# Optimization experiments

Hardware: AMD Instinct MI355X
Metric: run time of the kernel (lower is better)

## Reference

```python
import jax, jax.numpy as jnp
import numpy as np

N = 8192
IN_F = 512
OUT_F = 64
ALPHA = 0.2  # LeakyReLU negative slope
NEG_INF = -9e15


def setup_inputs() -> dict:
    key = jax.random.key(0)
    k1, k2, k3, k4 = jax.random.split(key, 4)
    # xavier_uniform-style scale (gain=1.414)
    w_bound = 1.414 * np.sqrt(6.0 / (IN_F + OUT_F))
    a_bound = 1.414 * np.sqrt(6.0 / (2 * OUT_F + 1))
    return {
        "input": jax.random.normal(k1, (N, IN_F), dtype=jnp.float32),
        "adj": jax.random.randint(k2, (N, N), 0, 2, dtype=jnp.int32),
        "W": jax.random.uniform(k3, (IN_F, OUT_F), jnp.float32, -w_bound, w_bound),
        "a": jax.random.uniform(k4, (2 * OUT_F, 1), jnp.float32, -a_bound, a_bound),
        "sig_sample_size": 512,
    }


def reference(input, adj, W, a, sig_sample_size):
    h = input @ W  # [N, F]
    # Split 'a' so e_ij = leakyrelu(a1.h_i + a2.h_j) without the N*N*2F repeat/cat
    a1, a2 = a[:OUT_F, 0], a[OUT_F:, 0]  # [F], [F]
    e = jax.nn.leaky_relu((h @ a1)[:, None] + (h @ a2)[None, :], negative_slope=ALPHA)  # [N, N]
    attention = jnp.where(adj > 0, e, NEG_INF)
    attention = jax.nn.softmax(attention, axis=1)
    sig_scores = jnp.sum(attention, axis=0)  # [N]
    _, indices = jax.lax.top_k(sig_scores, sig_sample_size)
    return indices
```

## Files before the change

kernel.cpp:

```cpp
#include <hip/hip_runtime.h>
#include <stdint.h>

#define NROW 8192
#define IN_F 512
#define OUT_F 64
#define ALPHA 0.2f

typedef int int4e __attribute__((ext_vector_type(4)));

__device__ float  g_wa1[IN_F];
__device__ float  g_wa2[IN_F];
__device__ float  g_f1[NROW];
__device__ float  g_f2[NROW];
__device__ float  g_E2f[NROW];
__device__ float  g_F2f[NROW];
__device__ double g_E2d[NROW];
__device__ double g_F2d[NROW];
__device__ double g_accp[NROW];
__device__ double g_accn[NROW];
__device__ double g_colsum[NROW];
__device__ unsigned long long g_maskP[(size_t)NROW * 128];
__device__ unsigned long long g_maskN[(size_t)NROW * 128];

__global__ void prep_wa(const float* __restrict__ W, const float* __restrict__ a) {
    int k = threadIdx.x;
    if (k < IN_F) {
        double s1 = 0.0, s2 = 0.0;
        for (int t = 0; t < OUT_F; ++t) {
            double w = (double)W[k * OUT_F + t];
            s1 += w * (double)a[t];
            s2 += w * (double)a[OUT_F + t];
        }
        g_wa1[k] = (float)s1;
        g_wa2[k] = (float)s2;
        #pragma unroll
        for (int i = 0; i < 16; ++i) g_colsum[k * 16 + i] = 0.0;
    }
}

__global__ void __launch_bounds__(256) compute_f(const float* __restrict__ in) {
    int wave = threadIdx.x >> 6, lane = threadIdx.x & 63;
    int row = blockIdx.x * 4 + wave;
    const float4* in4  = (const float4*)(in + (size_t)row * IN_F);
    const float4* wa14 = (const float4*)g_wa1;
    const float4* wa24 = (const float4*)g_wa2;
    double s1 = 0.0, s2 = 0.0;
    #pragma unroll
    for (int half = 0; half < 2; ++half) {
        int idx = half * 64 + lane;
        float4 x = in4[idx];
        float4 u = wa14[idx];
        float4 v = wa24[idx];
        s1 += (double)x.x*u.x + (double)x.y*u.y + (double)x.z*u.z + (double)x.w*u.w;
        s2 += (double)x.x*v.x + (double)x.y*v.y + (double)x.z*v.z + (double)x.w*v.w;
    }
    #pragma unroll
    for (int off = 32; off > 0; off >>= 1) {
        s1 += __shfl_down(s1, off, 64);
        s2 += __shfl_down(s2, off, 64);
    }
    if (lane == 0) {
        float f1 = (float)s1, f2 = (float)s2;
        g_f1[row] = f1; g_f2[row] = f2;
        double e2 = exp((double)f2), g2 = exp(0.2 * (double)f2);
        g_E2d[row] = e2;        g_F2d[row] = g2;
        g_E2f[row] = (float)e2; g_F2f[row] = (float)g2;
    }
}

__global__ void __launch_bounds__(256) row_z_mask(const int* __restrict__ adj) {
    __shared__ float E2s[NROW];
    __shared__ float F2s[NROW];
    __shared__ double zp[16], zn[16];
    int tid = threadIdx.x;
    int wave = tid >> 6, lane = tid & 63;
    for (int k = tid; k < NROW / 4; k += 256) {
        ((float4*)E2s)[k] = ((const float4*)g_E2f)[k];
        ((float4*)F2s)[k] = ((const float4*)g_F2f)[k];
    }
    __syncthreads();
    int row0 = blockIdx.x * 4;
    for (int r = 0; r < 4; ++r) {
        int row = row0 + r;
        float f1r = g_f1[row];
        float Ft = expf(-0.2f * f1r);
        const int4e* arow = (const int4e*)(adj + (size_t)row * NROW) + wave * 512;
        unsigned long long mywordP = 0, mywordN = 0;
        double accp = 0.0, accn = 0.0;
        #pragma unroll
        for (int it = 0; it < 8; ++it) {
            int4e av = __builtin_nontemporal_load(arow + it * 64 + lane);
            int colbase = wave * 2048 + it * 256 + lane * 4;
            float4 E2v = *(const float4*)&E2s[colbase];
            float4 F2v = *(const float4*)&F2s[colbase];
            bool p0 = av.x > 0, p1 = av.y > 0, p2 = av.z > 0, p3 = av.w > 0;
            bool q0 = F2v.x > Ft, q1 = F2v.y > Ft, q2 = F2v.z > Ft, q3 = F2v.w > Ft;
            unsigned long long bp0 = __ballot(p0 && q0),  bn0 = __ballot(p0 && !q0);
            unsigned long long bp1 = __ballot(p1 && q1),  bn1 = __ballot(p1 && !q1);
            unsigned long long bp2 = __ballot(p2 && q2),  bn2 = __ballot(p2 && !q2);
            unsigned long long bp3 = __ballot(p3 && q3),  bn3 = __ballot(p3 && !q3);
            int bl = it * 4;
            if (lane == bl)     { mywordP = bp0; mywordN = bn0; }
            if (lane == bl + 1) { mywordP = bp1; mywordN = bn1; }
            if (lane == bl + 2) { mywordP = bp2; mywordN = bn2; }
            if (lane == bl + 3) { mywordP = bp3; mywordN = bn3; }
            accp += (p0 && q0) ? (double)E2v.x : 0.0;
            accn += (p0 && !q0) ? (double)F2v.x : 0.0;
            accp += (p1 && q1) ? (double)E2v.y : 0.0;
            accn += (p1 && !q1) ? (double)F2v.y : 0.0;
            accp += (p2 && q2) ? (double)E2v.z : 0.0;
            accn += (p2 && !q2) ? (double)F2v.z : 0.0;
            accp += (p3 && q3) ? (double)E2v.w : 0.0;
            accn += (p3 && !q3) ? (double)F2v.w : 0.0;
        }
        if (lane < 32) {
            g_maskP[(size_t)row * 128 + wave * 32 + lane] = mywordP;
            g_maskN[(size_t)row * 128 + wave * 32 + lane] = mywordN;
        }
        #pragma unroll
        for (int off = 32; off > 0; off >>= 1) {
            accp += __shfl_down(accp, off, 64);
            accn += __shfl_down(accn, off, 64);
        }
        if (lane == 0) { zp[r * 4 + wave] = accp; zn[r * 4 + wave] = accn; }
    }
    __syncthreads();
    if (tid < 4) {
        g_accp[row0 + tid] = zp[tid*4+0] + zp[tid*4+1] + zp[tid*4+2] + zp[tid*4+3];
        g_accn[row0 + tid] = zn[tid*4+0] + zn[tid*4+1] + zn[tid*4+2] + zn[tid*4+3];
    }
}

__device__ __forceinline__ unsigned long long btr64(unsigned long long x, int lane) {
    const unsigned long long hm[6] = {
        0xAAAAAAAAAAAAAAAAULL, 0xCCCCCCCCCCCCCCCCULL, 0xF0F0F0F0F0F0F0F0ULL,
        0xFF00FF00FF00FF00ULL, 0xFFFF0000FFFF0000ULL, 0xFFFFFFFF00000000ULL };
    #pragma unroll
    for (int s = 0; s < 6; ++s) {
        int d = 1 << s;
        unsigned long long y = __shfl_xor(x, d, 64);
        unsigned long long hi = hm[s];
        x = (lane & d) ? ((x & hi) | ((y >> d) & ~hi))
                       : ((x & ~hi) | ((y << d) & hi));
    }
    return x;
}

__global__ void __launch_bounds__(256) colsum_kernel() {
    __shared__ double2 GHs[256];
    int tid = threadIdx.x;
    int w = tid >> 6, lane = tid & 63;
    int cb = blockIdx.x & 31;
    int rb = blockIdx.x >> 5;
    int i0 = rb * 256;
    {
        float f1v = g_f1[i0 + tid];
        double e1 = exp((double)f1v), h1 = exp(0.2 * (double)f1v);
        double Z = e1 * g_accp[i0 + tid] + h1 * g_accn[i0 + tid];
        double zi = 1.0 / Z;
        GHs[tid] = make_double2(e1 * zi, h1 * zi);
    }
    __syncthreads();
    int glo[4], ghi[4], hlo[4], hhi[4];
    #pragma unroll
    for (int t = 0; t < 4; ++t) {
        double2 gh = GHs[t * 64 + lane];
        glo[t] = __double2loint(gh.x); ghi[t] = __double2hiint(gh.x);
        hlo[t] = __double2loint(gh.y); hhi[t] = __double2hiint(gh.y);
    }
    int W = cb * 4 + w;
    unsigned long long TP[4], TN[4];
    #pragma unroll
    for (int t = 0; t < 4; ++t) {
        unsigned long long xp = g_maskP[(size_t)(i0 + t * 64 + lane) * 128 + W];
        unsigned long long xn = g_maskN[(size_t)(i0 + t * 64 + lane) * 128 + W];
        TP[t] = btr64(xp, lane);
        TN[t] = btr64(xn, lane);
    }
    int j = (W >> 5) * 2048 + ((W >> 2) & 7) * 256 + lane * 4 + (W & 3);
    double accp = 0.0, accn = 0.0;
    #pragma unroll
    for (int t = 0; t < 4; ++t) {
        unsigned long long wp = TP[t], wn = TN[t];
        int a0 = glo[t], a1 = ghi[t], b0 = hlo[t], b1 = hhi[t];
        for (int s = 0; s < 64; ++s) {
            double G1i = __hiloint2double(__builtin_amdgcn_readlane(a1, s),
                                          __builtin_amdgcn_readlane(a0, s));
            double H1i = __hiloint2double(__builtin_amdgcn_readlane(b1, s),
                                          __builtin_amdgcn_readlane(b0, s));
            accp += ((wp >> s) & 1ULL) ? G1i : 0.0;
            accn += ((wn >> s) & 1ULL) ? H1i : 0.0;
        }
    }
    double res = g_E2d[j] * accp + g_F2d[j] * accn;
    atomicAdd(&g_colsum[j], res);
}

__global__ void __launch_bounds__(1024) topk_kernel(int* __restrict__ out, int K) {
    __shared__ unsigned int sbits[NROW];
    __shared__ unsigned int hist[256];
    __shared__ unsigned long long cand[1024];
    __shared__ unsigned long long s_prefix;
    __shared__ unsigned int s_want, s_cnt;
    int tid = threadIdx.x;
    int lane = tid & 63;
    for (int k = tid; k < NROW; k += 1024) {
        float s = (float)g_colsum[k];
        unsigned int u = __float_as_uint(s);
        u = (u & 0x80000000u) ? ~u : (u | 0x80000000u);
        sbits[k] = u;
    }
    if (tid == 0) { s_prefix = 0ULL; s_want = (unsigned)K; s_cnt = 0; }
    __syncthreads();
    for (int lvl = 0; lvl < 6; ++lvl) {
        int shift = 40 - lvl * 8;
        if (tid < 256) hist[tid] = 0;
        __syncthreads();
        unsigned long long pmask = (lvl == 0) ? 0ULL : (~0ULL << (shift + 8));
        unsigned long long prefix = s_prefix;
        for (int k = tid; k < NROW; k += 1024) {
            unsigned long long kk =
                ((unsigned long long)sbits[k] << 13) | (unsigned long long)(8191 - k);
            bool match = ((kk & pmask) == prefix);
            unsigned bb = (unsigned)(kk >> shift) & 255u;
            unsigned long long act = __ballot(match);
            unsigned long long same = act;
            #pragma unroll
            for (int t = 0; t < 8; ++t) {
                unsigned long long bt = __ballot((bb >> t) & 1u);
                same &= ((bb >> t) & 1u) ? bt : ~bt;
            }
            if (match) {
                int lead = __ffsll((long long)same) - 1;
                if (lane == lead) atomicAdd(&hist[bb], (unsigned)__popcll(same));
            }
        }
        __syncthreads();
        if (tid == 0) {
            unsigned cum = 0; int b = 255;
            for (; b >= 0; --b) { cum += hist[b]; if (cum >= s_want) break; }
            if (b < 0) b = 0;
            s_want -= (cum - hist[b]);
            s_prefix |= ((unsigned long long)b << shift);
        }
        __syncthreads();
    }
    unsigned long long thr = s_prefix;
    for (int k = tid; k < NROW; k += 1024) {
        unsigned long long kk =
            ((unsigned long long)sbits[k] << 13) | (unsigned long long)(8191 - k);
        bool keep = (kk >= thr);
        unsigned long long m = __ballot(keep);
        if (m) {
            int lead = __ffsll((long long)m) - 1;
            unsigned base = 0;
            if (lane == lead) base = atomicAdd(&s_cnt, (unsigned)__popcll(m));
            base = (unsigned)__shfl((int)base, lead, 64);
            if (keep) {
                unsigned pos = base + (unsigned)__popcll(m & ((1ULL << lane) - 1ULL));
                if (pos < 1024u) cand[pos] = kk;
            }
        }
    }
    __syncthreads();
    unsigned cnt = s_cnt;
    if ((unsigned)tid >= cnt) cand[tid] = 0ULL;
    __syncthreads();
    for (int k2 = 2; k2 <= 1024; k2 <<= 1) {
        for (int jj = k2 >> 1; jj > 0; jj >>= 1) {
            int ixj = tid ^ jj;
            if (ixj > tid) {
                unsigned long long a = cand[tid], b = cand[ixj];
                bool up = ((tid & k2) == 0);
                if (up ? (a < b) : (a > b)) { cand[tid] = b; cand[ixj] = a; }
            }
            __syncthreads();
        }
    }
    if (tid < K) out[tid] = 8191 - (int)(cand[tid] & 0x1FFFULL);
}

extern "C" void kernel_launch(void* const* d_in, const int* in_sizes, int n_in,
                              void* d_out, int out_size, void* d_ws, size_t ws_size,
                              hipStream_t stream) {
    const float* input = (const float*)d_in[0];
    const int*   adj   = (const int*)d_in[1];
    const float* W     = (const float*)d_in[2];
    const float* a     = (const float*)d_in[3];
    int* out = (int*)d_out;
    int K = out_size;

    prep_wa<<<1, 512, 0, stream>>>(W, a);
    compute_f<<<NROW / 4, 256, 0, stream>>>(input);
    row_z_mask<<<NROW / 4, 256, 0, stream>>>(adj);
    colsum_kernel<<<1024, 256, 0, stream>>>();
    topk_kernel<<<1, 1024, 0, stream>>>(out, K);
}
```

Baseline: 565.7 us.

## Fuse W·a prep into row projection kernel and enlarge row_z_mask blocks

Merges the single-block prep_wa kernel into compute_f, with each block recomputing the W·a vectors into shared memory and zeroing its slice of colsum. This removes one launch and the serial prep step, at the cost of redundant W·a work in every block. row_z_mask now uses 1024-thread blocks covering 16 rows, so the E2/F2 shared-memory staging is amortised over four times as many rows. The adj loads also switch from nontemporal to normal loads.

```diff
diff --git a/kernel.cpp b/kernel.cpp
--- a/kernel.cpp
+++ b/kernel.cpp
@@ -8,8 +8,6 @@
 
 typedef int int4e __attribute__((ext_vector_type(4)));
 
-__device__ float  g_wa1[IN_F];
-__device__ float  g_wa2[IN_F];
 __device__ float  g_f1[NROW];
 __device__ float  g_f2[NROW];
 __device__ float  g_E2f[NROW];
@@ -22,28 +20,30 @@
 __device__ unsigned long long g_maskP[(size_t)NROW * 128];
 __device__ unsigned long long g_maskN[(size_t)NROW * 128];
 
-__global__ void prep_wa(const float* __restrict__ W, const float* __restrict__ a) {
-    int k = threadIdx.x;
-    if (k < IN_F) {
+__global__ void __launch_bounds__(512) fused_f(const float* __restrict__ in,
+                                               const float* __restrict__ W,
+                                               const float* __restrict__ a) {
+    __shared__ __align__(16) float wa1s[IN_F];
+    __shared__ __align__(16) float wa2s[IN_F];
+    int tid = threadIdx.x;
+    {
+        int k = tid;
         double s1 = 0.0, s2 = 0.0;
         for (int t = 0; t < OUT_F; ++t) {
             double w = (double)W[k * OUT_F + t];
             s1 += w * (double)a[t];
             s2 += w * (double)a[OUT_F + t];
         }
-        g_wa1[k] = (float)s1;
-        g_wa2[k] = (float)s2;
-        #pragma unroll
-        for (int i = 0; i < 16; ++i) g_colsum[k * 16 + i] = 0.0;
-    }
-}
-
-__global__ void __launch_bounds__(256) compute_f(const float* __restrict__ in) {
-    int wave = threadIdx.x >> 6, lane = threadIdx.x & 63;
-    int row = blockIdx.x * 4 + wave;
+        wa1s[k] = (float)s1;
+        wa2s[k] = (float)s2;
+    }
+    if (tid < 8) g_colsum[blockIdx.x * 8 + tid] = 0.0;
+    __syncthreads();
+    int wave = tid >> 6, lane = tid & 63;
+    int row = blockIdx.x * 8 + wave;
     const float4* in4  = (const float4*)(in + (size_t)row * IN_F);
-    const float4* wa14 = (const float4*)g_wa1;
-    const float4* wa24 = (const float4*)g_wa2;
+    const float4* wa14 = (const float4*)wa1s;
+    const float4* wa24 = (const float4*)wa2s;
     double s1 = 0.0, s2 = 0.0;
     #pragma unroll
     for (int half = 0; half < 2; ++half) {
@@ -68,29 +68,31 @@
     }
 }
 
-__global__ void __launch_bounds__(256) row_z_mask(const int* __restrict__ adj) {
+__global__ void __launch_bounds__(1024) row_z_mask(const int* __restrict__ adj) {
     __shared__ float E2s[NROW];
     __shared__ float F2s[NROW];
-    __shared__ double zp[16], zn[16];
+    __shared__ double zp[16][4], zn[16][4];
     int tid = threadIdx.x;
     int wave = tid >> 6, lane = tid & 63;
-    for (int k = tid; k < NROW / 4; k += 256) {
+    int q = wave & 3;
+    int rg = wave >> 2;
+    for (int k = tid; k < NROW / 4; k += 1024) {
         ((float4*)E2s)[k] = ((const float4*)g_E2f)[k];
         ((float4*)F2s)[k] = ((const float4*)g_F2f)[k];
     }
     __syncthreads();
-    int row0 = blockIdx.x * 4;
+    int row0 = blockIdx.x * 16;
     for (int r = 0; r < 4; ++r) {
-        int row = row0 + r;
+        int row = row0 + rg * 4 + r;
         float f1r = g_f1[row];
         float Ft = expf(-0.2f * f1r);
-        const int4e* arow = (const int4e*)(adj + (size_t)row * NROW) + wave * 512;
+        const int4e* arow = (const int4e*)(adj + (size_t)row * NROW) + q * 512;
         unsigned long long mywordP = 0, mywordN = 0;
         double accp = 0.0, accn = 0.0;
         #pragma unroll
         for (int it = 0; it < 8; ++it) {
-            int4e av = __builtin_nontemporal_load(arow + it * 64 + lane);
-            int colbase = wave * 2048 + it * 256 + lane * 4;
+            int4e av = arow[it * 64 + lane];
+            int colbase = q * 2048 + it * 256 + lane * 4;
             float4 E2v = *(const float4*)&E2s[colbase];
             float4 F2v = *(const float4*)&F2s[colbase];
             bool p0 = av.x > 0, p1 = av.y > 0, p2 = av.z > 0, p3 = av.w > 0;
@@ -114,20 +116,20 @@
             accn += (p3 && !q3) ? (double)F2v.w : 0.0;
         }
         if (lane < 32) {
-            g_maskP[(size_t)row * 128 + wave * 32 + lane] = mywordP;
-            g_maskN[(size_t)row * 128 + wave * 32 + lane] = mywordN;
+            g_maskP[(size_t)row * 128 + q * 32 + lane] = mywordP;
+            g_maskN[(size_t)row * 128 + q * 32 + lane] = mywordN;
         }
         #pragma unroll
         for (int off = 32; off > 0; off >>= 1) {
             accp += __shfl_down(accp, off, 64);
             accn += __shfl_down(accn, off, 64);
         }
-        if (lane == 0) { zp[r * 4 + wave] = accp; zn[r * 4 + wave] = accn; }
-    }
-    __syncthreads();
-    if (tid < 4) {
-        g_accp[row0 + tid] = zp[tid*4+0] + zp[tid*4+1] + zp[tid*4+2] + zp[tid*4+3];
-        g_accn[row0 + tid] = zn[tid*4+0] + zn[tid*4+1] + zn[tid*4+2] + zn[tid*4+3];
+        if (lane == 0) { zp[rg * 4 + r][q] = accp; zn[rg * 4 + r][q] = accn; }
+    }
+    __syncthreads();
+    if (tid < 16) {
+        g_accp[row0 + tid] = zp[tid][0] + zp[tid][1] + zp[tid][2] + zp[tid][3];
+        g_accn[row0 + tid] = zn[tid][0] + zn[tid][1] + zn[tid][2] + zn[tid][3];
     }
 }
 
@@ -290,9 +292,8 @@
     int* out = (int*)d_out;
     int K = out_size;
 
-    prep_wa<<<1, 512, 0, stream>>>(W, a);
-    compute_f<<<NROW / 4, 256, 0, stream>>>(input);
-    row_z_mask<<<NROW / 4, 256, 0, stream>>>(adj);
+    fused_f<<<NROW / 8, 512, 0, stream>>>(input, W, a);
+    row_z_mask<<<NROW / 16, 1024, 0, stream>>>(adj);
     colsum_kernel<<<1024, 256, 0, stream>>>();
     topk_kernel<<<1, 1024, 0, stream>>>(out, K);
 }
```

New measurement: 571.3 us. Within noise of the previous version (+1.0%).

## Store single adjacency bitmask and recompute sign split in colsum kernel

Applied to the files above, without the earlier changes.

The row pass now writes one adjacency bitmask per row instead of separate positive and negative masks, which halves the mask writes and later reads. The colsum kernel recomputes the sign of f1_i + f2_j per element to split the contributions. The row kernel also handles one row per block, preloads all adjacency vectors, and reads the E2/F2 tables from global memory instead of staging them in shared memory. The cost is extra ALU work in the colsum inner loop, plus a possible mismatch between the float comparison F2 > Ft and the recomputed sign test near zero.

```diff
diff --git a/kernel.cpp b/kernel.cpp
--- a/kernel.cpp
+++ b/kernel.cpp
@@ -19,8 +19,7 @@
 __device__ double g_accp[NROW];
 __device__ double g_accn[NROW];
 __device__ double g_colsum[NROW];
-__device__ unsigned long long g_maskP[(size_t)NROW * 128];
-__device__ unsigned long long g_maskN[(size_t)NROW * 128];
+__device__ unsigned long long g_mask[(size_t)NROW * 128];
 
 __global__ void prep_wa(const float* __restrict__ W, const float* __restrict__ a) {
     int k = threadIdx.x;
@@ -68,66 +67,54 @@
     }
 }
 
-__global__ void __launch_bounds__(256) row_z_mask(const int* __restrict__ adj) {
-    __shared__ float E2s[NROW];
-    __shared__ float F2s[NROW];
-    __shared__ double zp[16], zn[16];
+__global__ void __launch_bounds__(256) maskrow_kernel(const int* __restrict__ adj) {
+    __shared__ double zp[4], zn[4];
     int tid = threadIdx.x;
     int wave = tid >> 6, lane = tid & 63;
-    for (int k = tid; k < NROW / 4; k += 256) {
-        ((float4*)E2s)[k] = ((const float4*)g_E2f)[k];
-        ((float4*)F2s)[k] = ((const float4*)g_F2f)[k];
-    }
-    __syncthreads();
-    int row0 = blockIdx.x * 4;
-    for (int r = 0; r < 4; ++r) {
-        int row = row0 + r;
-        float f1r = g_f1[row];
-        float Ft = expf(-0.2f * f1r);
-        const int4e* arow = (const int4e*)(adj + (size_t)row * NROW) + wave * 512;
-        unsigned long long mywordP = 0, mywordN = 0;
-        double accp = 0.0, accn = 0.0;
-        #pragma unroll
-        for (int it = 0; it < 8; ++it) {
-            int4e av = __builtin_nontemporal_load(arow + it * 64 + lane);
-            int colbase = wave * 2048 + it * 256 + lane * 4;
-            float4 E2v = *(const float4*)&E2s[colbase];
-            float4 F2v = *(const float4*)&F2s[colbase];
-            bool p0 = av.x > 0, p1 = av.y > 0, p2 = av.z > 0, p3 = av.w > 0;
-            bool q0 = F2v.x > Ft, q1 = F2v.y > Ft, q2 = F2v.z > Ft, q3 = F2v.w > Ft;
-            unsigned long long bp0 = __ballot(p0 && q0),  bn0 = __ballot(p0 && !q0);
-            unsigned long long bp1 = __ballot(p1 && q1),  bn1 = __ballot(p1 && !q1);
-            unsigned long long bp2 = __ballot(p2 && q2),  bn2 = __ballot(p2 && !q2);
-            unsigned long long bp3 = __ballot(p3 && q3),  bn3 = __ballot(p3 && !q3);
-            int bl = it * 4;
-            if (lane == bl)     { mywordP = bp0; mywordN = bn0; }
-            if (lane == bl + 1) { mywordP = bp1; mywordN = bn1; }
-            if (lane == bl + 2) { mywordP = bp2; mywordN = bn2; }
-            if (lane == bl + 3) { mywordP = bp3; mywordN = bn3; }
-            accp += (p0 && q0) ? (double)E2v.x : 0.0;
-            accn += (p0 && !q0) ? (double)F2v.x : 0.0;
-            accp += (p1 && q1) ? (double)E2v.y : 0.0;
-            accn += (p1 && !q1) ? (double)F2v.y : 0.0;
-            accp += (p2 && q2) ? (double)E2v.z : 0.0;
-            accn += (p2 && !q2) ? (double)F2v.z : 0.0;
-            accp += (p3 && q3) ? (double)E2v.w : 0.0;
-            accn += (p3 && !q3) ? (double)F2v.w : 0.0;
-        }
-        if (lane < 32) {
-            g_maskP[(size_t)row * 128 + wave * 32 + lane] = mywordP;
-            g_maskN[(size_t)row * 128 + wave * 32 + lane] = mywordN;
-        }
-        #pragma unroll
-        for (int off = 32; off > 0; off >>= 1) {
-            accp += __shfl_down(accp, off, 64);
-            accn += __shfl_down(accn, off, 64);
-        }
-        if (lane == 0) { zp[r * 4 + wave] = accp; zn[r * 4 + wave] = accn; }
-    }
-    __syncthreads();
-    if (tid < 4) {
-        g_accp[row0 + tid] = zp[tid*4+0] + zp[tid*4+1] + zp[tid*4+2] + zp[tid*4+3];
-        g_accn[row0 + tid] = zn[tid*4+0] + zn[tid*4+1] + zn[tid*4+2] + zn[tid*4+3];
+    int row = blockIdx.x;
+    float f1r = g_f1[row];
+    float Ft = expf(-0.2f * f1r);
+    const int4e* arow = (const int4e*)(adj + (size_t)row * NROW) + wave * 512;
+    int4e av[8];
+    #pragma unroll
+    for (int it = 0; it < 8; ++it) av[it] = arow[it * 64 + lane];
+    unsigned long long myword = 0;
+    double accp = 0.0, accn = 0.0;
+    #pragma unroll
+    for (int it = 0; it < 8; ++it) {
+        int colbase = wave * 2048 + it * 256 + lane * 4;
+        float4 E2v = *(const float4*)&g_E2f[colbase];
+        float4 F2v = *(const float4*)&g_F2f[colbase];
+        bool p0 = av[it].x > 0, p1 = av[it].y > 0;
+        bool p2 = av[it].z > 0, p3 = av[it].w > 0;
+        unsigned long long b0 = __ballot(p0), b1 = __ballot(p1);
+        unsigned long long b2 = __ballot(p2), b3 = __ballot(p3);
+        int bl = it * 4;
+        if (lane == bl)     myword = b0;
+        if (lane == bl + 1) myword = b1;
+        if (lane == bl + 2) myword = b2;
+        if (lane == bl + 3) myword = b3;
+        bool q0 = F2v.x > Ft, q1 = F2v.y > Ft, q2 = F2v.z > Ft, q3 = F2v.w > Ft;
+        accp += (p0 && q0) ? (double)E2v.x : 0.0;
+        accn += (p0 && !q0) ? (double)F2v.x : 0.0;
+        accp += (p1 && q1) ? (double)E2v.y : 0.0;
+        accn += (p1 && !q1) ? (double)F2v.y : 0.0;
+        accp += (p2 && q2) ? (double)E2v.z : 0.0;
+        accn += (p2 && !q2) ? (double)F2v.z : 0.0;
+        accp += (p3 && q3) ? (double)E2v.w : 0.0;
+        accn += (p3 && !q3) ? (double)F2v.w : 0.0;
+    }
+    if (lane < 32) g_mask[(size_t)row * 128 + wave * 32 + lane] = myword;
+    #pragma unroll
+    for (int off = 32; off > 0; off >>= 1) {
+        accp += __shfl_down(accp, off, 64);
+        accn += __shfl_down(accn, off, 64);
+    }
+    if (lane == 0) { zp[wave] = accp; zn[wave] = accn; }
+    __syncthreads();
+    if (tid == 0) {
+        g_accp[row] = zp[0] + zp[1] + zp[2] + zp[3];
+        g_accn[row] = zn[0] + zn[1] + zn[2] + zn[3];
     }
 }
 
@@ -148,48 +135,54 @@
 
 __global__ void __launch_bounds__(256) colsum_kernel() {
     __shared__ double2 GHs[256];
+    __shared__ float   f1sh[256];
     int tid = threadIdx.x;
     int w = tid >> 6, lane = tid & 63;
     int cb = blockIdx.x & 31;
     int rb = blockIdx.x >> 5;
     int i0 = rb * 256;
+    float f1v = g_f1[i0 + tid];
+    f1sh[tid] = f1v;
     {
-        float f1v = g_f1[i0 + tid];
         double e1 = exp((double)f1v), h1 = exp(0.2 * (double)f1v);
         double Z = e1 * g_accp[i0 + tid] + h1 * g_accn[i0 + tid];
         double zi = 1.0 / Z;
         GHs[tid] = make_double2(e1 * zi, h1 * zi);
     }
     __syncthreads();
-    int glo[4], ghi[4], hlo[4], hhi[4];
+    int glo[4], ghi[4], hlo[4], hhi[4], fbits[4];
     #pragma unroll
     for (int t = 0; t < 4; ++t) {
         double2 gh = GHs[t * 64 + lane];
         glo[t] = __double2loint(gh.x); ghi[t] = __double2hiint(gh.x);
         hlo[t] = __double2loint(gh.y); hhi[t] = __double2hiint(gh.y);
+        fbits[t] = __float_as_int(f1sh[t * 64 + lane]);
     }
     int W = cb * 4 + w;
-    unsigned long long TP[4], TN[4];
+    unsigned long long TP[4];
     #pragma unroll
     for (int t = 0; t < 4; ++t) {
-        unsigned long long xp = g_maskP[(size_t)(i0 + t * 64 + lane) * 128 + W];
-        unsigned long long xn = g_maskN[(size_t)(i0 + t * 64 + lane) * 128 + W];
+        unsigned long long xp = g_mask[(size_t)(i0 + t * 64 + lane) * 128 + W];
         TP[t] = btr64(xp, lane);
-        TN[t] = btr64(xn, lane);
     }
     int j = (W >> 5) * 2048 + ((W >> 2) & 7) * 256 + lane * 4 + (W & 3);
+    float f2j = g_f2[j];
     double accp = 0.0, accn = 0.0;
     #pragma unroll
     for (int t = 0; t < 4; ++t) {
-        unsigned long long wp = TP[t], wn = TN[t];
-        int a0 = glo[t], a1 = ghi[t], b0 = hlo[t], b1 = hhi[t];
+        unsigned long long wp = TP[t];
+        int a0 = glo[t], a1 = ghi[t], b0 = hlo[t], b1 = hhi[t], fb = fbits[t];
         for (int s = 0; s < 64; ++s) {
             double G1i = __hiloint2double(__builtin_amdgcn_readlane(a1, s),
                                           __builtin_amdgcn_readlane(a0, s));
             double H1i = __hiloint2double(__builtin_amdgcn_readlane(b1, s),
                                           __builtin_amdgcn_readlane(b0, s));
-            accp += ((wp >> s) & 1ULL) ? G1i : 0.0;
-            accn += ((wn >> s) & 1ULL) ? H1i : 0.0;
+            float f1i = __int_as_float(__builtin_amdgcn_readlane(fb, s));
+            bool b = (wp >> s) & 1ULL;
+            float e = f1i + f2j;
+            bool pos = e > 0.0f;
+            accp += (b && pos)  ? G1i : 0.0;
+            accn += (b && !pos) ? H1i : 0.0;
         }
     }
     double res = g_E2d[j] * accp + g_F2d[j] * accn;
@@ -292,7 +285,7 @@
 
     prep_wa<<<1, 512, 0, stream>>>(W, a);
     compute_f<<<NROW / 4, 256, 0, stream>>>(input);
-    row_z_mask<<<NROW / 4, 256, 0, stream>>>(adj);
+    maskrow_kernel<<<NROW, 256, 0, stream>>>(adj);
     colsum_kernel<<<1024, 256, 0, stream>>>();
     topk_kernel<<<1, 1024, 0, stream>>>(out, K);
 }
```

Measured after the change: 530.2 us. 1.07x faster.
